# Optimization experiments

Hardware: AMD Instinct MI355X
Metric: run time of the kernel (lower is better)

Reference implementation:

```python
import jax, jax.numpy as jnp
import numpy as np

B, L, D, H, NL, F, VOCAB = 16, 2048, 768, 12, 4, 32, 2362
HD = D // H          # head dim = 64
DFF = D              # feed_forward_dimensions = n_embd in the builder
EPS = 1e-6           # fast_transformers linear attention eps


def setup_inputs() -> dict:
    key = jax.random.key(0)
    ks = jax.random.split(key, 16)
    def nrm(k, shape, s=0.02):
        return jax.random.normal(k, shape, dtype=jnp.float32) * s
    return {
        "idx": jax.random.randint(ks[0], (B, L), 0, VOCAB, dtype=jnp.int32),
        "mask": jnp.ones((B, L), dtype=jnp.int32),
        "tok_emb": nrm(ks[1], (VOCAB, D)),
        "Wq": nrm(ks[2], (NL, D, D)), "bq": jnp.zeros((NL, D), jnp.float32),
        "Wk": nrm(ks[3], (NL, D, D)), "bk": jnp.zeros((NL, D), jnp.float32),
        "Wv": nrm(ks[4], (NL, D, D)), "bv": jnp.zeros((NL, D), jnp.float32),
        "Wo": nrm(ks[5], (NL, D, D)), "bo": jnp.zeros((NL, D), jnp.float32),
        # GeneralizedRandomFeatures random projection, one per layer (builder redraws per layer)
        "omega": jax.random.normal(ks[6], (NL, HD, F), dtype=jnp.float32),
        "W1": nrm(ks[7], (NL, D, DFF)), "b1": jnp.zeros((NL, DFF), jnp.float32),
        "W2": nrm(ks[8], (NL, DFF, D)), "b2": jnp.zeros((NL, D), jnp.float32),
        "g1": jnp.ones((NL, D), jnp.float32), "be1": jnp.zeros((NL, D), jnp.float32),
        "g2": jnp.ones((NL, D), jnp.float32), "be2": jnp.zeros((NL, D), jnp.float32),
        "gf": jnp.ones((D,), jnp.float32), "bf": jnp.zeros((D,), jnp.float32),
    }


def _layernorm(x, g, b):
    mu = jnp.mean(x, -1, keepdims=True)
    var = jnp.mean(jnp.square(x - mu), -1, keepdims=True)
    return (x - mu) * jax.lax.rsqrt(var + 1e-5) * g + b


def _rotary(x):
    # x: [B, L, H, HD]; MolFormer rotary: x*cos + rotate_half(x)*sin
    half = HD // 2
    inv = 1.0 / (10000.0 ** (jnp.arange(0, HD, 2, dtype=jnp.float32) / HD))
    t = jnp.arange(x.shape[1], dtype=jnp.float32)
    fr = t[:, None] * inv[None, :]                 # [L, HD/2]
    emb = jnp.concatenate([fr, fr], -1)            # [L, HD]
    cos = jnp.cos(emb)[None, :, None, :]
    sin = jnp.sin(emb)[None, :, None, :]
    x1, x2 = x[..., :half], x[..., half:]
    rot = jnp.concatenate([-x2, x1], -1)
    return x * cos + rot * sin


def _linear_attn(x, keymask, Wq, bq, Wk, bk, Wv, bv, Wo, bo, omega):
    b, l = x.shape[0], x.shape[1]
    q = (x @ Wq + bq).reshape(b, l, H, HD)
    k = (x @ Wk + bk).reshape(b, l, H, HD)
    v = (x @ Wv + bv).reshape(b, l, H, HD)
    q = _rotary(q)
    k = _rotary(k)
    # GeneralizedRandomFeatures: phi(x) = relu(x @ omega)
    phq = jax.nn.relu(jnp.einsum('blhd,df->blhf', q, omega))
    phk = jax.nn.relu(jnp.einsum('blhd,df->blhf', k, omega))
    phk = phk * keymask[:, :, None, None]
    # associative linear attention: Q (K^T V) with normalizer
    kv = jnp.einsum('blhf,blhd->bhfd', phk, v)          # [B,H,F,HD]
    z = 1.0 / (jnp.einsum('blhf,bhf->blh', phq, phk.sum(1)) + EPS)
    out = jnp.einsum('blhf,bhfd,blh->blhd', phq, kv, z)
    return out.reshape(b, l, D) @ Wo + bo


def reference(idx, mask, tok_emb, Wq, bq, Wk, bk, Wv, bv, Wo, bo, omega,
              W1, b1, W2, b2, g1, be1, g2, be2, gf, bf):
    keymask = mask.astype(jnp.float32)
    x = tok_emb[idx]                                    # [B,L,D]
    for i in range(NL):
        y = _linear_attn(x, keymask, Wq[i], bq[i], Wk[i], bk[i],
                         Wv[i], bv[i], Wo[i], bo[i], omega[i])
        x = x + y                                       # dropout = 0 (eval)
        y = x = _layernorm(x, g1[i], be1[i])
        y = jax.nn.gelu(y @ W1[i] + b1[i], approximate=False)
        y = y @ W2[i] + b2[i]
        x = _layernorm(x + y, g2[i], be2[i])
    return _layernorm(x, gf, bf)
```

## Files before the change

kernel.cpp:

```cpp
#include <hip/hip_runtime.h>
#include <math.h>

#define Bsz 16
#define Lseq 2048
#define Dm 768
#define Hn 12
#define HDim 64
#define Fdim 32
#define NLayers 4
#define NTOK (Bsz * Lseq)
#define NSPLIT 16

typedef __bf16 bf16;
typedef bf16 bf16x8 __attribute__((ext_vector_type(8)));
typedef float f32x4 __attribute__((ext_vector_type(4)));

#define AS1(p) ((__attribute__((address_space(1))) void*)(uintptr_t)(p))
#define AS3(p) ((__attribute__((address_space(3))) void*)(p))

__global__ __launch_bounds__(256) void wconv_kernel(const float* __restrict__ W,
                                                    bf16* __restrict__ Wt) {
  __shared__ float t[32][33];
  int l = blockIdx.z;
  int kb = blockIdx.y * 32, nb = blockIdx.x * 32;
  const float* Wl = W + (size_t)l * Dm * Dm;
  bf16* Wtl = Wt + (size_t)l * Dm * Dm;
  int tx = threadIdx.x, ty = threadIdx.y;
#pragma unroll
  for (int i = 0; i < 32; i += 8)
    t[ty + i][tx] = Wl[(size_t)(kb + ty + i) * Dm + nb + tx];
  __syncthreads();
#pragma unroll
  for (int i = 0; i < 32; i += 8)
    Wtl[(size_t)(nb + ty + i) * Dm + kb + tx] = (bf16)t[tx][ty + i];
}

__global__ __launch_bounds__(256) void gemm_mfma_kernel(
    const bf16* __restrict__ A, const bf16* __restrict__ Wt,
    const float* __restrict__ bias, bf16* __restrict__ C, int act, int rot) {
  const int K = Dm, N = Dm;
  __shared__ bf16 As[128 * 32];
  __shared__ bf16 Bs[128 * 32];
  const int tid = threadIdx.x;
  const int lane = tid & 63;
  const int wave = tid >> 6;
  const int wr = (wave >> 1) << 6;
  const int wc = (wave & 1) << 6;
  const int m0 = blockIdx.y << 7;
  const int n0 = blockIdx.x << 7;
  const int c0 = tid, c1 = tid + 256;
  const bf16* a0 = A + (size_t)(m0 + (c0 >> 2)) * K + ((c0 & 3) << 3);
  const bf16* a1 = A + (size_t)(m0 + (c1 >> 2)) * K + ((c1 & 3) << 3);
  const bf16* b0 = Wt + (size_t)(n0 + (c0 >> 2)) * K + ((c0 & 3) << 3);
  const bf16* b1 = Wt + (size_t)(n0 + (c1 >> 2)) * K + ((c1 & 3) << 3);
  bf16* const As0 = As + c0 * 8;
  bf16* const As1 = As + c1 * 8;
  bf16* const Bs0 = Bs + c0 * 8;
  bf16* const Bs1 = Bs + c1 * 8;

  const int la = lane & 15, qd = lane >> 4;
  const int aoff = (wr + la) * 32 + qd * 8;
  const int boff = (wc + la) * 32 + qd * 8;

  f32x4 acc[4][4] = {};

  for (int k0 = 0; k0 < K; k0 += 32) {
    __builtin_amdgcn_global_load_lds(AS1(a0 + k0), AS3(As0), 16, 0, 0);
    __builtin_amdgcn_global_load_lds(AS1(a1 + k0), AS3(As1), 16, 0, 0);
    __builtin_amdgcn_global_load_lds(AS1(b0 + k0), AS3(Bs0), 16, 0, 0);
    __builtin_amdgcn_global_load_lds(AS1(b1 + k0), AS3(Bs1), 16, 0, 0);
    __syncthreads();
    bf16x8 af[4], bfr[4];
#pragma unroll
    for (int i = 0; i < 4; ++i) af[i] = *(const bf16x8*)(As + aoff + i * 512);
#pragma unroll
    for (int j = 0; j < 4; ++j) bfr[j] = *(const bf16x8*)(Bs + boff + j * 512);
#pragma unroll
    for (int i = 0; i < 4; ++i)
#pragma unroll
      for (int j = 0; j < 4; ++j)
        acc[i][j] = __builtin_amdgcn_mfma_f32_16x16x32_bf16(af[i], bfr[j],
                                                            acc[i][j], 0, 0, 0);
    __syncthreads();
  }

  if (!rot) {
#pragma unroll
    for (int i = 0; i < 4; ++i) {
      int rbase = m0 + wr + i * 16 + qd * 4;
#pragma unroll
      for (int j = 0; j < 4; ++j) {
        int col = n0 + wc + j * 16 + la;
        float bc = bias[col];
#pragma unroll
        for (int r = 0; r < 4; ++r) {
          float v = acc[i][j][r] + bc;
          if (act) v = 0.5f * v * (1.0f + erff(v * 0.70710678118654752f));
          C[(size_t)(rbase + r) * N + col] = (bf16)v;
        }
      }
    }
  } else {
#pragma unroll
    for (int i = 0; i < 4; ++i) {
      int rbase = m0 + wr + i * 16 + qd * 4;
#pragma unroll
      for (int jj = 0; jj < 2; ++jj) {
        int d = jj * 16 + la;
        int col1 = n0 + wc + d;
        int col2 = col1 + 32;
        float b1c = bias[col1], b2c = bias[col2];
        float inv = expf(-(float)d * (9.210340371976184f / 32.0f));
#pragma unroll
        for (int r = 0; r < 4; ++r) {
          int row = rbase + r;
          int l = row & (Lseq - 1);
          float fr = (float)l * inv;
          float s, c;
          sincosf(fr, &s, &c);
          float x1 = acc[i][jj][r] + b1c;
          float x2 = acc[i][jj + 2][r] + b2c;
          C[(size_t)row * N + col1] = (bf16)(x1 * c - x2 * s);
          C[(size_t)row * N + col2] = (bf16)(x2 * c + x1 * s);
        }
      }
    }
  }
}

__global__ __launch_bounds__(256) void embed_kernel(
    const int* __restrict__ idx, const float* __restrict__ emb,
    float* __restrict__ Xf, bf16* __restrict__ Xb) {
  int o = blockIdx.x * 256 + threadIdx.x;
  int t = o / Dm, d = o - t * Dm;
  float v = emb[(size_t)idx[t] * Dm + d];
  Xf[o] = v;
  Xb[o] = (bf16)v;
}

__global__ __launch_bounds__(256) void phi_mfma_kernel(
    const bf16* __restrict__ qk, const float* __restrict__ omega,
    const int* __restrict__ mask, bf16* __restrict__ ph) {
  __shared__ bf16 omT[32][72];
  int tid = threadIdx.x;
  for (int i = tid; i < HDim * Fdim; i += 256) {
    int d = i >> 5, f = i & 31;
    omT[f][d] = (bf16)omega[i];
  }
  __syncthreads();
  const int h = blockIdx.y;
  const int lane = tid & 63, wave = tid >> 6;
  const int la = lane & 15, qd = lane >> 4;
  const int t0 = blockIdx.x * 256 + wave * 64;
  const bf16* qbase = qk + (size_t)t0 * Dm + h * HDim;

  bf16x8 bfr[2][2];
#pragma unroll
  for (int j = 0; j < 2; ++j)
#pragma unroll
    for (int ks = 0; ks < 2; ++ks)
      bfr[j][ks] = *(const bf16x8*)(&omT[j * 16 + la][ks * 32 + qd * 8]);

  f32x4 acc[4][2] = {};
#pragma unroll
  for (int ks = 0; ks < 2; ++ks) {
    bf16x8 af[4];
#pragma unroll
    for (int i = 0; i < 4; ++i)
      af[i] = *(const bf16x8*)(qbase + (size_t)(i * 16 + la) * Dm + ks * 32 +
                               qd * 8);
#pragma unroll
    for (int i = 0; i < 4; ++i)
#pragma unroll
      for (int j = 0; j < 2; ++j)
        acc[i][j] = __builtin_amdgcn_mfma_f32_16x16x32_bf16(af[i], bfr[j][ks],
                                                            acc[i][j], 0, 0, 0);
  }
#pragma unroll
  for (int i = 0; i < 4; ++i) {
#pragma unroll
    for (int r = 0; r < 4; ++r) {
      int row = t0 + i * 16 + qd * 4 + r;
      float mm = mask ? (float)mask[row] : 1.0f;
#pragma unroll
      for (int j = 0; j < 2; ++j) {
        float val = fmaxf(acc[i][j][r], 0.0f) * mm;
        ph[(size_t)row * (Hn * Fdim) + h * Fdim + j * 16 + la] = (bf16)val;
      }
    }
  }
}

__global__ __launch_bounds__(256) void kvsum_kernel(
    const bf16* __restrict__ phk, const bf16* __restrict__ v,
    float* __restrict__ kvp, float* __restrict__ ksump) {
  const int bh = blockIdx.x;
  const int b = bh / Hn, h = bh - b * Hn;
  const int s = blockIdx.y;
  const int tid = threadIdx.x;
  const int f = tid >> 3, d0 = (tid & 7) << 3;
  const int lbeg = s * (Lseq / NSPLIT);
  const bf16* pp =
      phk + (size_t)(b * Lseq + lbeg) * (Hn * Fdim) + h * Fdim + f;
  const bf16* vp = v + (size_t)(b * Lseq + lbeg) * Dm + h * HDim + d0;
  float acc[8] = {};
  float ks = 0.0f;
#pragma unroll 4
  for (int l = 0; l < Lseq / NSPLIT; ++l) {
    float p = (float)pp[(size_t)l * (Hn * Fdim)];
    bf16x8 vv = *(const bf16x8*)(vp + (size_t)l * Dm);
    ks += p;
#pragma unroll
    for (int q = 0; q < 8; ++q) acc[q] = fmaf(p, (float)vv[q], acc[q]);
  }
  float* o = kvp + (size_t)(s * (Bsz * Hn) + bh) * (Fdim * HDim) + tid * 8;
  f32x4 lo = {acc[0], acc[1], acc[2], acc[3]};
  f32x4 hi = {acc[4], acc[5], acc[6], acc[7]};
  *(f32x4*)o = lo;
  *(f32x4*)(o + 4) = hi;
  if ((tid & 7) == 0)
    ksump[(size_t)(s * (Bsz * Hn) + bh) * Fdim + f] = ks;
}

__global__ __launch_bounds__(256) void kvreduce_kernel(
    const float* __restrict__ kvp, const float* __restrict__ ksump,
    float* __restrict__ kv, float* __restrict__ ksum) {
  const int idx = blockIdx.x * 256 + threadIdx.x;
  float a = 0.0f;
#pragma unroll
  for (int s = 0; s < NSPLIT; ++s)
    a += kvp[(size_t)s * (Bsz * Hn * Fdim * HDim) + idx];
  kv[idx] = a;
  if (idx < Bsz * Hn * Fdim) {
    float k2 = 0.0f;
#pragma unroll
    for (int s = 0; s < NSPLIT; ++s)
      k2 += ksump[(size_t)s * (Bsz * Hn * Fdim) + idx];
    ksum[idx] = k2;
  }
}

__global__ __launch_bounds__(256) void zden_kernel(
    const bf16* __restrict__ phq, const float* __restrict__ ksum,
    float* __restrict__ zr) {
  int idx = blockIdx.x * 256 + threadIdx.x;
  int h = idx % Hn;
  int b = idx / (Lseq * Hn);
  const bf16* pq = phq + (size_t)idx * Fdim;
  const float* ks = ksum + ((size_t)b * Hn + h) * Fdim;
  float acc = 0.0f;
#pragma unroll
  for (int f = 0; f < Fdim; ++f) acc = fmaf((float)pq[f], ks[f], acc);
  zr[idx] = 1.0f / (acc + 1e-6f);
}

__global__ __launch_bounds__(256) void attn_mfma_kernel(
    const bf16* __restrict__ phq, const float* __restrict__ kv,
    const float* __restrict__ zr, bf16* __restrict__ out) {
  __shared__ bf16 kvb[64 * 40];
  int bh = blockIdx.y;
  int b = bh / Hn, h = bh - b * Hn;
  int tid = threadIdx.x, lane = tid & 63, wave = tid >> 6;
  {
    int d = tid >> 2, f0 = (tid & 3) << 3;
    const float* src = kv + ((size_t)bh * Fdim + f0) * HDim + d;
    bf16x8 tmp;
#pragma unroll
    for (int q = 0; q < 8; ++q) tmp[q] = (bf16)src[(size_t)q * HDim];
    *(bf16x8*)(kvb + d * 40 + f0) = tmp;
  }
  __syncthreads();
  const int la = lane & 15, qd = lane >> 4;
  const int t0 = b * Lseq + blockIdx.x * 256 + wave * 64;
  bf16x8 bfr[4];
#pragma unroll
  for (int jt = 0; jt < 4; ++jt)
    bfr[jt] = *(const bf16x8*)(kvb + (jt * 16 + la) * 40 + qd * 8);
  bf16x8 af[4];
#pragma unroll
  for (int i = 0; i < 4; ++i)
    af[i] = *(const bf16x8*)(phq +
                             ((size_t)(t0 + i * 16 + la) * Hn + h) * Fdim +
                             qd * 8);
  f32x4 acc[4][4] = {};
#pragma unroll
  for (int i = 0; i < 4; ++i)
#pragma unroll
    for (int jt = 0; jt < 4; ++jt)
      acc[i][jt] = __builtin_amdgcn_mfma_f32_16x16x32_bf16(af[i], bfr[jt],
                                                           acc[i][jt], 0, 0, 0);
#pragma unroll
  for (int i = 0; i < 4; ++i) {
    int rbase = t0 + i * 16 + qd * 4;
#pragma unroll
    for (int r = 0; r < 4; ++r) {
      float z = zr[(size_t)(rbase + r) * Hn + h];
#pragma unroll
      for (int jt = 0; jt < 4; ++jt)
        out[(size_t)(rbase + r) * Dm + h * HDim + jt * 16 + la] =
            (bf16)(acc[i][jt][r] * z);
    }
  }
}

__global__ __launch_bounds__(256) void ln_residual_kernel(
    const bf16* __restrict__ y, const float* __restrict__ xres,
    const float* __restrict__ g, const float* __restrict__ be,
    float* __restrict__ xf_out, bf16* __restrict__ xb_out) {
  __shared__ float red[8];
  int t = blockIdx.x, tid = threadIdx.x;
  int lane = tid & 63, wave = tid >> 6;
  const bf16* yr = y + (size_t)t * Dm;
  const float* xr = xres + (size_t)t * Dm;
  float v0 = xr[tid] + (float)yr[tid];
  float v1 = xr[tid + 256] + (float)yr[tid + 256];
  float v2 = xr[tid + 512] + (float)yr[tid + 512];
  float s = v0 + v1 + v2;
#pragma unroll
  for (int off = 32; off > 0; off >>= 1) s += __shfl_xor(s, off, 64);
  if (lane == 0) red[wave] = s;
  __syncthreads();
  float mu = (red[0] + red[1] + red[2] + red[3]) * (1.0f / 768.0f);
  float d0 = v0 - mu, d1 = v1 - mu, d2 = v2 - mu;
  float s2 = d0 * d0 + d1 * d1 + d2 * d2;
#pragma unroll
  for (int off = 32; off > 0; off >>= 1) s2 += __shfl_xor(s2, off, 64);
  if (lane == 0) red[4 + wave] = s2;
  __syncthreads();
  float rs =
      rsqrtf((red[4] + red[5] + red[6] + red[7]) * (1.0f / 768.0f) + 1e-5f);
  float o0 = d0 * rs * g[tid] + be[tid];
  float o1 = d1 * rs * g[tid + 256] + be[tid + 256];
  float o2 = d2 * rs * g[tid + 512] + be[tid + 512];
  float* xo = xf_out + (size_t)t * Dm;
  bf16* bo = xb_out + (size_t)t * Dm;
  xo[tid] = o0;
  xo[tid + 256] = o1;
  xo[tid + 512] = o2;
  bo[tid] = (bf16)o0;
  bo[tid + 256] = (bf16)o1;
  bo[tid + 512] = (bf16)o2;
}

__global__ __launch_bounds__(256) void ln_final_kernel(
    const float* __restrict__ x, const float* __restrict__ g,
    const float* __restrict__ be, float* __restrict__ out) {
  __shared__ float red[8];
  int t = blockIdx.x, tid = threadIdx.x;
  int lane = tid & 63, wave = tid >> 6;
  const float* xr = x + (size_t)t * Dm;
  float v0 = xr[tid], v1 = xr[tid + 256], v2 = xr[tid + 512];
  float s = v0 + v1 + v2;
#pragma unroll
  for (int off = 32; off > 0; off >>= 1) s += __shfl_xor(s, off, 64);
  if (lane == 0) red[wave] = s;
  __syncthreads();
  float mu = (red[0] + red[1] + red[2] + red[3]) * (1.0f / 768.0f);
  float d0 = v0 - mu, d1 = v1 - mu, d2 = v2 - mu;
  float s2 = d0 * d0 + d1 * d1 + d2 * d2;
#pragma unroll
  for (int off = 32; off > 0; off >>= 1) s2 += __shfl_xor(s2, off, 64);
  if (lane == 0) red[4 + wave] = s2;
  __syncthreads();
  float rs =
      rsqrtf((red[4] + red[5] + red[6] + red[7]) * (1.0f / 768.0f) + 1e-5f);
  float* outr = out + (size_t)t * Dm;
  outr[tid] = d0 * rs * g[tid] + be[tid];
  outr[tid + 256] = d1 * rs * g[tid + 256] + be[tid + 256];
  outr[tid + 512] = d2 * rs * g[tid + 512] + be[tid + 512];
}

extern "C" void kernel_launch(void* const* d_in, const int* in_sizes, int n_in,
                              void* d_out, int out_size, void* d_ws,
                              size_t ws_size, hipStream_t stream) {
  const int* idx = (const int*)d_in[0];
  const int* mask = (const int*)d_in[1];
  const float* tok_emb = (const float*)d_in[2];
  const float* Wq = (const float*)d_in[3];
  const float* bq = (const float*)d_in[4];
  const float* Wk = (const float*)d_in[5];
  const float* bk = (const float*)d_in[6];
  const float* Wv = (const float*)d_in[7];
  const float* bv = (const float*)d_in[8];
  const float* Wo = (const float*)d_in[9];
  const float* bo = (const float*)d_in[10];
  const float* omega = (const float*)d_in[11];
  const float* W1 = (const float*)d_in[12];
  const float* b1 = (const float*)d_in[13];
  const float* W2 = (const float*)d_in[14];
  const float* b2 = (const float*)d_in[15];
  const float* g1 = (const float*)d_in[16];
  const float* be1 = (const float*)d_in[17];
  const float* g2 = (const float*)d_in[18];
  const float* be2 = (const float*)d_in[19];
  const float* gf = (const float*)d_in[20];
  const float* bf = (const float*)d_in[21];

  const size_t TD = (size_t)NTOK * Dm;
  const size_t WSZ = (size_t)NLayers * Dm * Dm;
  bf16* wsb = (bf16*)d_ws;
  bf16* WqT = wsb;
  bf16* WkT = WqT + WSZ;
  bf16* WvT = WkT + WSZ;
  bf16* WoT = WvT + WSZ;
  bf16* W1T = WoT + WSZ;
  bf16* W2T = W1T + WSZ;
  float* Xf = (float*)(wsb + 6 * WSZ);
  bf16* Ab = (bf16*)(Xf + TD);
  float* KV = (float*)(Ab + TD);
  float* KSUM = KV + (size_t)Bsz * Hn * Fdim * HDim;
  float* ZR = KSUM + (size_t)Bsz * Hn * Fdim;
  bf16* Xb = (bf16*)d_out;
  bf16* PHQ = Xb + TD;
  bf16* PHK = PHQ + (size_t)NTOK * Hn * Fdim;
  bf16* Yb = PHQ;
  float* KVP = (float*)d_out;
  float* KSUMP = KVP + (size_t)NSPLIT * Bsz * Hn * Fdim * HDim;

  dim3 wg(Dm / 32, Dm / 32, NLayers), wb(32, 8);
  wconv_kernel<<<wg, wb, 0, stream>>>(Wq, WqT);
  wconv_kernel<<<wg, wb, 0, stream>>>(Wk, WkT);
  wconv_kernel<<<wg, wb, 0, stream>>>(Wv, WvT);
  wconv_kernel<<<wg, wb, 0, stream>>>(Wo, WoT);
  wconv_kernel<<<wg, wb, 0, stream>>>(W1, W1T);
  wconv_kernel<<<wg, wb, 0, stream>>>(W2, W2T);

  dim3 gg(Dm / 128, NTOK / 128), gb(256);
  dim3 kvg(Bsz * Hn, NSPLIT);
  dim3 ag(Lseq / 256, Bsz * Hn);
  dim3 pg(NTOK / 256, Hn);
  const int elem_grid = (NTOK * Dm) / 256;
  const int zden_grid = (NTOK * Hn) / 256;
  const int kvr_grid = (Bsz * Hn * Fdim * HDim) / 256;

  embed_kernel<<<elem_grid, 256, 0, stream>>>(idx, tok_emb, Xf, Xb);

  for (int i = 0; i < NLayers; ++i) {
    const size_t wo = (size_t)i * Dm * Dm;
    const size_t bo_ = (size_t)i * Dm;
    const float* omi = omega + (size_t)i * HDim * Fdim;

    gemm_mfma_kernel<<<gg, gb, 0, stream>>>(Xb, WqT + wo, bq + bo_, Ab, 0, 1);
    phi_mfma_kernel<<<pg, 256, 0, stream>>>(Ab, omi, nullptr, PHQ);
    gemm_mfma_kernel<<<gg, gb, 0, stream>>>(Xb, WkT + wo, bk + bo_, Ab, 0, 1);
    phi_mfma_kernel<<<pg, 256, 0, stream>>>(Ab, omi, mask, PHK);
    gemm_mfma_kernel<<<gg, gb, 0, stream>>>(Xb, WvT + wo, bv + bo_, Ab, 0, 0);
    kvsum_kernel<<<kvg, 256, 0, stream>>>(PHK, Ab, KVP, KSUMP);
    kvreduce_kernel<<<kvr_grid, 256, 0, stream>>>(KVP, KSUMP, KV, KSUM);
    zden_kernel<<<zden_grid, 256, 0, stream>>>(PHQ, KSUM, ZR);
    attn_mfma_kernel<<<ag, 256, 0, stream>>>(PHQ, KV, ZR, Ab);
    gemm_mfma_kernel<<<gg, gb, 0, stream>>>(Ab, WoT + wo, bo + bo_, Yb, 0, 0);
    ln_residual_kernel<<<NTOK, 256, 0, stream>>>(Yb, Xf, g1 + bo_, be1 + bo_,
                                                 Xf, Xb);
    gemm_mfma_kernel<<<gg, gb, 0, stream>>>(Xb, W1T + wo, b1 + bo_, Ab, 1, 0);
    gemm_mfma_kernel<<<gg, gb, 0, stream>>>(Ab, W2T + wo, b2 + bo_, Yb, 0, 0);
    ln_residual_kernel<<<NTOK, 256, 0, stream>>>(Yb, Xf, g2 + bo_, be2 + bo_,
                                                 Xf, Xb);
  }
  ln_final_kernel<<<NTOK, 256, 0, stream>>>(Xf, gf, bf, (float*)d_out);
}
```

Baseline: 2.945 ms.

## Double-buffer GEMM LDS tiles and remap block indices for cache locality

```diff
diff --git a/kernel.cpp b/kernel.cpp
--- a/kernel.cpp
+++ b/kernel.cpp
@@ -39,24 +39,22 @@
     const bf16* __restrict__ A, const bf16* __restrict__ Wt,
     const float* __restrict__ bias, bf16* __restrict__ C, int act, int rot) {
   const int K = Dm, N = Dm;
-  __shared__ bf16 As[128 * 32];
-  __shared__ bf16 Bs[128 * 32];
+  __shared__ bf16 As[2][128 * 32];
+  __shared__ bf16 Bs[2][128 * 32];
   const int tid = threadIdx.x;
   const int lane = tid & 63;
   const int wave = tid >> 6;
   const int wr = (wave >> 1) << 6;
   const int wc = (wave & 1) << 6;
-  const int m0 = blockIdx.y << 7;
-  const int n0 = blockIdx.x << 7;
+  const int hw = blockIdx.y * gridDim.x + blockIdx.x;
+  const int lt = (hw & 7) * 192 + (hw >> 3);
+  const int n0 = (lt % 6) << 7;
+  const int m0 = (lt / 6) << 7;
   const int c0 = tid, c1 = tid + 256;
   const bf16* a0 = A + (size_t)(m0 + (c0 >> 2)) * K + ((c0 & 3) << 3);
   const bf16* a1 = A + (size_t)(m0 + (c1 >> 2)) * K + ((c1 & 3) << 3);
   const bf16* b0 = Wt + (size_t)(n0 + (c0 >> 2)) * K + ((c0 & 3) << 3);
   const bf16* b1 = Wt + (size_t)(n0 + (c1 >> 2)) * K + ((c1 & 3) << 3);
-  bf16* const As0 = As + c0 * 8;
-  bf16* const As1 = As + c1 * 8;
-  bf16* const Bs0 = Bs + c0 * 8;
-  bf16* const Bs1 = Bs + c1 * 8;
 
   const int la = lane & 15, qd = lane >> 4;
   const int aoff = (wr + la) * 32 + qd * 8;
@@ -64,25 +62,49 @@
 
   f32x4 acc[4][4] = {};
 
-  for (int k0 = 0; k0 < K; k0 += 32) {
-    __builtin_amdgcn_global_load_lds(AS1(a0 + k0), AS3(As0), 16, 0, 0);
-    __builtin_amdgcn_global_load_lds(AS1(a1 + k0), AS3(As1), 16, 0, 0);
-    __builtin_amdgcn_global_load_lds(AS1(b0 + k0), AS3(Bs0), 16, 0, 0);
-    __builtin_amdgcn_global_load_lds(AS1(b1 + k0), AS3(Bs1), 16, 0, 0);
-    __syncthreads();
-    bf16x8 af[4], bfr[4];
-#pragma unroll
-    for (int i = 0; i < 4; ++i) af[i] = *(const bf16x8*)(As + aoff + i * 512);
-#pragma unroll
-    for (int j = 0; j < 4; ++j) bfr[j] = *(const bf16x8*)(Bs + boff + j * 512);
-#pragma unroll
-    for (int i = 0; i < 4; ++i)
-#pragma unroll
-      for (int j = 0; j < 4; ++j)
-        acc[i][j] = __builtin_amdgcn_mfma_f32_16x16x32_bf16(af[i], bfr[j],
-                                                            acc[i][j], 0, 0, 0);
-    __syncthreads();
-  }
+#define STAGE(buf, k0)                                                        \
+  do {                                                                        \
+    __builtin_amdgcn_global_load_lds(AS1(a0 + (k0)), AS3(&As[buf][c0 * 8]),   \
+                                     16, 0, 0);                               \
+    __builtin_amdgcn_global_load_lds(AS1(a1 + (k0)), AS3(&As[buf][c1 * 8]),   \
+                                     16, 0, 0);                               \
+    __builtin_amdgcn_global_load_lds(AS1(b0 + (k0)), AS3(&Bs[buf][c0 * 8]),   \
+                                     16, 0, 0);                               \
+    __builtin_amdgcn_global_load_lds(AS1(b1 + (k0)), AS3(&Bs[buf][c1 * 8]),   \
+                                     16, 0, 0);                               \
+  } while (0)
+
+#define COMPUTE(buf)                                                          \
+  do {                                                                        \
+    bf16x8 af[4], bfr[4];                                                     \
+    _Pragma("unroll") for (int i = 0; i < 4; ++i) af[i] =                     \
+        *(const bf16x8*)(&As[buf][aoff + i * 512]);                           \
+    _Pragma("unroll") for (int j = 0; j < 4; ++j) bfr[j] =                    \
+        *(const bf16x8*)(&Bs[buf][boff + j * 512]);                           \
+    _Pragma("unroll") for (int i = 0; i < 4; ++i)                             \
+        _Pragma("unroll") for (int j = 0; j < 4; ++j) acc[i][j] =             \
+            __builtin_amdgcn_mfma_f32_16x16x32_bf16(af[i], bfr[j],            \
+                                                    acc[i][j], 0, 0, 0);      \
+  } while (0)
+
+  STAGE(0, 0);
+  int cur = 0;
+  for (int t = 0; t < K / 32 - 1; ++t) {
+    STAGE(cur ^ 1, (t + 1) * 32);
+    asm volatile("s_waitcnt vmcnt(4)" ::: "memory");
+    __builtin_amdgcn_s_barrier();
+    __builtin_amdgcn_sched_barrier(0);
+    COMPUTE(cur);
+    __builtin_amdgcn_s_barrier();
+    __builtin_amdgcn_sched_barrier(0);
+    cur ^= 1;
+  }
+  asm volatile("s_waitcnt vmcnt(0)" ::: "memory");
+  __builtin_amdgcn_s_barrier();
+  __builtin_amdgcn_sched_barrier(0);
+  COMPUTE(cur);
+#undef STAGE
+#undef COMPUTE
 
   if (!rot) {
 #pragma unroll
```

After: 2.916 ms. About the same (-1.0%).

## Rework GEMM into 256x128 tile triple-buffered pipeline with swizzled LDS

Applied to the files above, without the earlier changes.

```diff
diff --git a/kernel.cpp b/kernel.cpp
--- a/kernel.cpp
+++ b/kernel.cpp
@@ -35,62 +35,137 @@
     Wtl[(size_t)(nb + ty + i) * Dm + kb + tx] = (bf16)t[tx][ty + i];
 }
 
-__global__ __launch_bounds__(256) void gemm_mfma_kernel(
+__global__ __launch_bounds__(512, 2) void gemm_mfma_kernel(
     const bf16* __restrict__ A, const bf16* __restrict__ Wt,
     const float* __restrict__ bias, bf16* __restrict__ C, int act, int rot) {
   const int K = Dm, N = Dm;
-  __shared__ bf16 As[128 * 32];
-  __shared__ bf16 Bs[128 * 32];
+  constexpr int BM = 256, BN = 128, BK = 64, NBUF = 3;
+  __shared__ bf16 As[NBUF][BM * BK];
+  __shared__ bf16 Bs[NBUF][BN * BK];
   const int tid = threadIdx.x;
   const int lane = tid & 63;
   const int wave = tid >> 6;
-  const int wr = (wave >> 1) << 6;
-  const int wc = (wave & 1) << 6;
-  const int m0 = blockIdx.y << 7;
-  const int n0 = blockIdx.x << 7;
-  const int c0 = tid, c1 = tid + 256;
-  const bf16* a0 = A + (size_t)(m0 + (c0 >> 2)) * K + ((c0 & 3) << 3);
-  const bf16* a1 = A + (size_t)(m0 + (c1 >> 2)) * K + ((c1 & 3) << 3);
-  const bf16* b0 = Wt + (size_t)(n0 + (c0 >> 2)) * K + ((c0 & 3) << 3);
-  const bf16* b1 = Wt + (size_t)(n0 + (c1 >> 2)) * K + ((c1 & 3) << 3);
-  bf16* const As0 = As + c0 * 8;
-  bf16* const As1 = As + c1 * 8;
-  bf16* const Bs0 = Bs + c0 * 8;
-  bf16* const Bs1 = Bs + c1 * 8;
+  const int wm = wave >> 1;
+  const int wn = wave & 1;
+  const int hw = blockIdx.y * gridDim.x + blockIdx.x;
+  const int lt = (hw & 7) * 96 + (hw >> 3);
+  const int n0 = (lt % 6) * BN;
+  const int m0 = (lt / 6) * BM;
 
   const int la = lane & 15, qd = lane >> 4;
-  const int aoff = (wr + la) * 32 + qd * 8;
-  const int boff = (wc + la) * 32 + qd * 8;
+
+  const bf16* aps[4];
+  int alds[4];
+#pragma unroll
+  for (int r = 0; r < 4; ++r) {
+    int s = r * 512 + tid;
+    int row = s >> 3, cpos = s & 7;
+    aps[r] = A + (size_t)(m0 + row) * K + ((cpos ^ (row & 7)) << 3);
+    alds[r] = s * 8;
+  }
+  const bf16* bps[2];
+  int blds[2];
+#pragma unroll
+  for (int r = 0; r < 2; ++r) {
+    int s = r * 512 + tid;
+    int row = s >> 3, cpos = s & 7;
+    bps[r] = Wt + (size_t)(n0 + row) * K + ((cpos ^ (row & 7)) << 3);
+    blds[r] = s * 8;
+  }
+
+  int abase[4], am7[4];
+#pragma unroll
+  for (int i = 0; i < 4; ++i) {
+    int row = wm * 64 + i * 16 + la;
+    abase[i] = row * BK;
+    am7[i] = row & 7;
+  }
+  int bbase[4], bm7[4];
+#pragma unroll
+  for (int j = 0; j < 4; ++j) {
+    int row = wn * 64 + j * 16 + la;
+    bbase[j] = row * BK;
+    bm7[j] = row & 7;
+  }
 
   f32x4 acc[4][4] = {};
 
-  for (int k0 = 0; k0 < K; k0 += 32) {
-    __builtin_amdgcn_global_load_lds(AS1(a0 + k0), AS3(As0), 16, 0, 0);
-    __builtin_amdgcn_global_load_lds(AS1(a1 + k0), AS3(As1), 16, 0, 0);
-    __builtin_amdgcn_global_load_lds(AS1(b0 + k0), AS3(Bs0), 16, 0, 0);
-    __builtin_amdgcn_global_load_lds(AS1(b1 + k0), AS3(Bs1), 16, 0, 0);
-    __syncthreads();
-    bf16x8 af[4], bfr[4];
-#pragma unroll
-    for (int i = 0; i < 4; ++i) af[i] = *(const bf16x8*)(As + aoff + i * 512);
-#pragma unroll
-    for (int j = 0; j < 4; ++j) bfr[j] = *(const bf16x8*)(Bs + boff + j * 512);
-#pragma unroll
-    for (int i = 0; i < 4; ++i)
-#pragma unroll
-      for (int j = 0; j < 4; ++j)
-        acc[i][j] = __builtin_amdgcn_mfma_f32_16x16x32_bf16(af[i], bfr[j],
-                                                            acc[i][j], 0, 0, 0);
-    __syncthreads();
-  }
+#define STAGE_P0(bufx, k0)                                                   \
+  do {                                                                       \
+    __builtin_amdgcn_global_load_lds(AS1(aps[0] + (k0)),                     \
+                                     AS3(&As[bufx][alds[0]]), 16, 0, 0);     \
+    __builtin_amdgcn_global_load_lds(AS1(aps[1] + (k0)),                     \
+                                     AS3(&As[bufx][alds[1]]), 16, 0, 0);     \
+    __builtin_amdgcn_global_load_lds(AS1(aps[2] + (k0)),                     \
+                                     AS3(&As[bufx][alds[2]]), 16, 0, 0);     \
+  } while (0)
+#define STAGE_P1(bufx, k0)                                                   \
+  do {                                                                       \
+    __builtin_amdgcn_global_load_lds(AS1(aps[3] + (k0)),                     \
+                                     AS3(&As[bufx][alds[3]]), 16, 0, 0);     \
+    __builtin_amdgcn_global_load_lds(AS1(bps[0] + (k0)),                     \
+                                     AS3(&Bs[bufx][blds[0]]), 16, 0, 0);     \
+    __builtin_amdgcn_global_load_lds(AS1(bps[1] + (k0)),                     \
+                                     AS3(&Bs[bufx][blds[1]]), 16, 0, 0);     \
+  } while (0)
+
+#define PHASE(bufx, ks)                                                      \
+  do {                                                                       \
+    bf16x8 af[4], bfr[4];                                                    \
+    _Pragma("unroll") for (int i = 0; i < 4; ++i) af[i] =                    \
+        *(const bf16x8*)(&As[bufx][abase[i] +                                \
+                                   ((((ks)*4 + qd) ^ am7[i]) << 3)]);        \
+    _Pragma("unroll") for (int j = 0; j < 4; ++j) bfr[j] =                   \
+        *(const bf16x8*)(&Bs[bufx][bbase[j] +                                \
+                                   ((((ks)*4 + qd) ^ bm7[j]) << 3)]);        \
+    __builtin_amdgcn_s_barrier();                                            \
+    __builtin_amdgcn_sched_barrier(0);                                       \
+    __builtin_amdgcn_s_setprio(1);                                           \
+    _Pragma("unroll") for (int i = 0; i < 4; ++i)                            \
+        _Pragma("unroll") for (int j = 0; j < 4; ++j) acc[i][j] =            \
+            __builtin_amdgcn_mfma_f32_16x16x32_bf16(af[i], bfr[j],           \
+                                                    acc[i][j], 0, 0, 0);     \
+    __builtin_amdgcn_s_setprio(0);                                           \
+  } while (0)
+
+  STAGE_P0(0, 0);
+  STAGE_P1(0, 0);
+  STAGE_P0(1, BK);
+  STAGE_P1(1, BK);
+  asm volatile("s_waitcnt vmcnt(6)" ::: "memory");
+  __builtin_amdgcn_s_barrier();
+  __builtin_amdgcn_sched_barrier(0);
+
+  const int NT = K / BK;
+  int bufc = 0, bufn = 2;
+  for (int t = 0; t < NT; ++t) {
+    const bool st = (t + 2) < NT;
+    if (st) STAGE_P0(bufn, (t + 2) * BK);
+    PHASE(bufc, 0);
+    if (st) STAGE_P1(bufn, (t + 2) * BK);
+    PHASE(bufc, 1);
+    if (t < NT - 1) {
+      if (st)
+        asm volatile("s_waitcnt vmcnt(6)" ::: "memory");
+      else
+        asm volatile("s_waitcnt vmcnt(0)" ::: "memory");
+      __builtin_amdgcn_s_barrier();
+      __builtin_amdgcn_sched_barrier(0);
+    }
+    bufc = (bufc + 1 == NBUF) ? 0 : bufc + 1;
+    bufn = (bufn + 1 == NBUF) ? 0 : bufn + 1;
+  }
+#undef STAGE_P0
+#undef STAGE_P1
+#undef PHASE
 
   if (!rot) {
 #pragma unroll
     for (int i = 0; i < 4; ++i) {
-      int rbase = m0 + wr + i * 16 + qd * 4;
+      int rbase = m0 + wm * 64 + i * 16 + qd * 4;
 #pragma unroll
       for (int j = 0; j < 4; ++j) {
-        int col = n0 + wc + j * 16 + la;
+        int col = n0 + wn * 64 + j * 16 + la;
         float bc = bias[col];
 #pragma unroll
         for (int r = 0; r < 4; ++r) {
@@ -103,11 +178,11 @@
   } else {
 #pragma unroll
     for (int i = 0; i < 4; ++i) {
-      int rbase = m0 + wr + i * 16 + qd * 4;
+      int rbase = m0 + wm * 64 + i * 16 + qd * 4;
 #pragma unroll
       for (int jj = 0; jj < 2; ++jj) {
         int d = jj * 16 + la;
-        int col1 = n0 + wc + d;
+        int col1 = n0 + wn * 64 + d;
         int col2 = col1 + 32;
         float b1c = bias[col1], b2c = bias[col2];
         float inv = expf(-(float)d * (9.210340371976184f / 32.0f));
@@ -425,7 +500,7 @@
   wconv_kernel<<<wg, wb, 0, stream>>>(W1, W1T);
   wconv_kernel<<<wg, wb, 0, stream>>>(W2, W2T);
 
-  dim3 gg(Dm / 128, NTOK / 128), gb(256);
+  dim3 gg(Dm / 128, NTOK / 256), gb(512);
   dim3 kvg(Bsz * Hn, NSPLIT);
   dim3 ag(Lseq / 256, Bsz * Hn);
   dim3 pg(NTOK / 256, Hn);
```

Result: faster. 2.559 ms (-13.1%).
